# Performance work log

Measured on AMD Instinct MI355X. Metric: run time of the kernel, lower is better.

Reference implementation:

```python
import jax, jax.numpy as jnp
import numpy as np

VOCAB = 50257
D = 256
N_BUBBLES = 64
N_EQ_STEPS = 5
SEQ_LEN = 1024
ETA = 0.1          # relaxation rate of the equilibrium solve
EPS = 1e-10        # eigenvalue clamp for the output distribution


def setup_inputs() -> dict:
    key = jax.random.key(0)
    k1, k2, k3 = jax.random.split(key, 3)
    tokens = jax.random.randint(k1, (SEQ_LEN,), 0, VOCAB)
    embed = jax.random.normal(k2, (VOCAB, D), dtype=jnp.float32) * 0.02
    bubbles = jax.random.normal(k3, (N_BUBBLES, D), dtype=jnp.float32)
    memory_decay = jnp.asarray(0.8, dtype=jnp.float32)
    return {"tokens": tokens, "embed": embed, "bubbles": bubbles,
            "memory_decay": memory_decay}


def _foam_step(memory, x, bubbles, decay):
    # memory: [N_BUBBLES, D], x: [D]
    x_with_memory = x + decay * memory.mean(axis=0)            # [D]
    # equilibrium solve: fixed small number of relaxation iterations
    s = bubbles                                                # [N_BUBBLES, D]
    for _ in range(N_EQ_STEPS):
        mean_field = s.mean(axis=0, keepdims=True)             # [1, D]
        s = s + ETA * (x_with_memory[None, :] - s) + ETA * (mean_field - s)
    # density matrix from equilibrium bubble states
    rho = (s.T @ s) / N_BUBBLES                                # [D, D]
    rho = rho / jnp.trace(rho)
    evals = jnp.linalg.eigvalsh(rho)                           # [D]
    dist = jnp.clip(evals, EPS)
    dist = dist / dist.sum()
    surface_tension = ((s - s.mean(axis=0, keepdims=True)) ** 2).mean()
    memory_new = decay * memory + (1.0 - decay) * s
    return memory_new, dist, surface_tension


def reference(tokens, embed, bubbles, memory_decay):
    decay = jax.nn.sigmoid(memory_decay)
    xs = embed[tokens]                                         # [SEQ_LEN, D]

    def scan_fn(mem, x):
        mem, dist, st = _foam_step(mem, x, bubbles, decay)
        return mem, (dist, st)

    mem0 = jnp.zeros((N_BUBBLES, D), dtype=jnp.float32)
    _, (dists, sts) = jax.lax.scan(scan_fn, mem0, xs)
    # per-step eigenvalue distributions of rho: [SEQ_LEN, D]
    return dists
```

## Files before the change

kernel.cpp:

```cpp
#include <hip/hip_runtime.h>
#include <hip/hip_bf16.h>
#include <math.h>

#define N_B   64
#define DIM   256
#define SEQ   1024
#define CF    0.32768f
#define CF2   0.1073741824f
#define BETA  0.59049f
#define EPSC  1e-10f
#define NSWEEP 3
#define ROUNDS (NSWEEP*63)

#define OFF_BMEAN 16
#define OFF_DT    (OFF_BMEAN + DIM)
#define OFF_DDT   (OFF_DT + DIM*N_B)
#define OFF_M     (OFF_DDT + N_B*N_B)

__global__ __launch_bounds__(256) void prep_kernel(const float* __restrict__ bubbles,
                                                   const float* __restrict__ mdecay,
                                                   float* __restrict__ ws) {
    int d = threadIdx.x;
    float s = 0.f;
    for (int b = 0; b < N_B; ++b) s += bubbles[b*DIM + d];
    float bm = s * (1.f/64.f);
    ws[OFF_BMEAN + d] = bm;
    float sq = 0.f;
    for (int b = 0; b < N_B; ++b) {
        float v = bubbles[b*DIM + d] - bm;
        ws[OFF_DT + d*N_B + b] = v;
        sq += v*v;
    }
    __shared__ float red[256];
    red[d] = sq;
    __syncthreads();
    for (int o = 128; o > 0; o >>= 1) {
        if (d < o) red[d] += red[d+o];
        __syncthreads();
    }
    if (d == 0) {
        ws[1] = red[0];
        ws[0] = 1.f/(1.f + expf(-mdecay[0]));
    }
}

__global__ __launch_bounds__(64) void ddt_kernel(float* __restrict__ ws) {
    const float* Dt = ws + OFF_DT;
    int i = blockIdx.x, j = threadIdx.x;
    __shared__ float coli[DIM];
    #pragma unroll
    for (int kk = 0; kk < 4; ++kk) coli[j + 64*kk] = Dt[(j + 64*kk)*N_B + i];
    __syncthreads();
    float acc = 0.f;
    #pragma unroll 8
    for (int k = 0; k < DIM; ++k) acc += coli[k] * Dt[k*N_B + j];
    ws[OFF_DDT + i*64 + j] = acc;
}

__global__ __launch_bounds__(256) void scan_kernel(const int* __restrict__ tokens,
                                                   const float* __restrict__ embed,
                                                   float* __restrict__ ws) {
    int d = threadIdx.x;
    float decay = ws[0];
    float bm = ws[OFF_BMEAN + d];
    const float omd = 1.f - decay;
    const float omb = 1.f - BETA;
    float mu = 0.f;
    for (int t0 = 0; t0 < SEQ; t0 += 16) {
        float x[16];
        #pragma unroll
        for (int u = 0; u < 16; ++u)
            x[u] = embed[tokens[t0+u]*DIM + d];
        #pragma unroll
        for (int u = 0; u < 16; ++u) {
            float xwm = x[u] + decay*mu;
            float m = BETA*bm + omb*xwm;
            ws[OFF_M + (t0+u)*DIM + d] = m;
            mu = decay*mu + omd*m;
        }
    }
}

__device__ __forceinline__ int triaddr(int i, int j) {
    int mn = min(i, j), mx = max(i, j);
    return mn*65 + mx;
}

__device__ __forceinline__ void tri_decomp(int L, int& a, int& b) {
    int a_ = 0, S = 0;
    while (S + (31 - a_) <= L) { S += 31 - a_; ++a_; }
    a = a_; b = a_ + 1 + (L - S);
}

#define SLOT_INIT(k, p, q, f) { f = ((k) == 0); p = f ? 63 : (k); q = f ? 0 : (63 - (k)); }
#define SLOT_ADV(p, q, f)     { if (!(f)) p = (p == 62) ? 0 : p + 1; q = (q == 62) ? 0 : q + 1; }

__global__ __launch_bounds__(256) void step_kernel(const float* __restrict__ ws,
                                                   float* __restrict__ out) {
    const int t    = blockIdx.x;
    const int tid  = threadIdx.x;
    const int lane = tid & 63;
    const int w    = tid >> 6;

    __shared__ float A[64][65];
    __shared__ float yv[64];
    __shared__ float ml[DIM];
    __shared__ float2 cs[32];
    __shared__ float ypart[4][64];
    __shared__ float wpart[4];
    __shared__ float sorted[64];

    float* Ad = &A[0][0];
    const float* Dt  = ws + OFF_DT;
    const float* DDT = ws + OFF_DDT;
    const float* m   = ws + OFF_M + (size_t)t*DIM;

    float mv = m[tid];
    ml[tid] = mv;
    float pp = mv*mv;
    #pragma unroll
    for (int o = 1; o < 64; o <<= 1) pp += __shfl_xor(pp, o);
    if (lane == 0) wpart[w] = pp;
    __syncthreads();
    const float mm2 = wpart[0]+wpart[1]+wpart[2]+wpart[3];

    {
        float acc = 0.f;
        const float* DtB = Dt + (w*64)*N_B + lane;
        #pragma unroll 8
        for (int kk = 0; kk < 64; ++kk) acc += DtB[kk*N_B] * ml[w*64 + kk];
        ypart[w][lane] = acc;
    }
    __syncthreads();
    if (tid < 64) yv[tid] = ypart[0][tid]+ypart[1][tid]+ypart[2][tid]+ypart[3][tid];
    __syncthreads();

    const float trDD = ws[1];
    const float tr   = mm2 + (CF2/64.f)*trDD;
    const float inv  = 1.f/(64.f*tr);

    {
        int i  = tid >> 2;
        int jb = (tid & 3) * 16;
        const float4* dd = (const float4*)(DDT + i*64 + jb);
        float yi = yv[i];
        #pragma unroll
        for (int u = 0; u < 4; ++u) {
            float4 d4 = dd[u];
            int j = jb + u*4;
            A[i][j+0] = (mm2 + CF*(yi + yv[j+0]) + CF2*d4.x) * inv;
            A[i][j+1] = (mm2 + CF*(yi + yv[j+1]) + CF2*d4.y) * inv;
            A[i][j+2] = (mm2 + CF*(yi + yv[j+2]) + CF2*d4.z) * inv;
            A[i][j+3] = (mm2 + CF*(yi + yv[j+3]) + CF2*d4.w) * inv;
        }
    }
    __syncthreads();

    const bool active = (tid < 248);

    int kr0 = 0, kc0 = 1, kr1 = 0, kc1 = 1;
    if (active) { tri_decomp(2*tid, kr0, kc0); tri_decomp(2*tid+1, kr1, kc1); }

    int pr0, qr0, pc0, qc0, pr1, qr1, pc1, qc1;
    bool fr0, fc0, fr1, fc1;
    SLOT_INIT(kr0, pr0, qr0, fr0);
    SLOT_INIT(kc0, pc0, qc0, fc0);
    SLOT_INIT(kr1, pr1, qr1, fr1);
    SLOT_INIT(kc1, pc1, qc1, fc1);

    int pA = 63, qA = 0; bool fA;
    if (tid < 32) SLOT_INIT(tid, pA, qA, fA);

    for (int rr = 0; rr < ROUNDS; ++rr) {
        if (tid < 32) {
            int aqp = triaddr(pA, qA);
            float app = Ad[pA*65 + pA];
            float aqq = Ad[qA*65 + qA];
            float apq = Ad[aqp];
            float ccf = 1.f, ssf = 0.f, ttf = 0.f;
            if (fabsf(apq) > 1e-36f) {
                float tau = (aqq - app)/(2.f*apq);
                ttf = 1.f/(fabsf(tau) + sqrtf(1.f + tau*tau));
                if (tau < 0.f) ttf = -ttf;
                ccf = rsqrtf(1.f + ttf*ttf);
                ssf = ttf*ccf;
            }
            cs[tid] = make_float2(ccf, ssf);
            Ad[pA*65 + pA] = app - ttf*apq;
            Ad[qA*65 + qA] = aqq + ttf*apq;
            Ad[aqp] = 0.f;
        }
        __syncthreads();

        if (active) {
            {
                float2 cr = cs[kr0], cc2 = cs[kc0];
                int a00 = triaddr(pr0, pc0), a01 = triaddr(pr0, qc0);
                int a10 = triaddr(qr0, pc0), a11 = triaddr(qr0, qc0);
                float x00 = Ad[a00], x01 = Ad[a01], x10 = Ad[a10], x11 = Ad[a11];
                float t0x = cc2.x*x00 - cc2.y*x01, t0y = cc2.y*x00 + cc2.x*x01;
                float t1x = cc2.x*x10 - cc2.y*x11, t1y = cc2.y*x10 + cc2.x*x11;
                Ad[a00] = cr.x*t0x - cr.y*t1x;
                Ad[a01] = cr.x*t0y - cr.y*t1y;
                Ad[a10] = cr.y*t0x + cr.x*t1x;
                Ad[a11] = cr.y*t0y + cr.x*t1y;
            }
            {
                float2 cr = cs[kr1], cc2 = cs[kc1];
                int a00 = triaddr(pr1, pc1), a01 = triaddr(pr1, qc1);
                int a10 = triaddr(qr1, pc1), a11 = triaddr(qr1, qc1);
                float x00 = Ad[a00], x01 = Ad[a01], x10 = Ad[a10], x11 = Ad[a11];
                float t0x = cc2.x*x00 - cc2.y*x01, t0y = cc2.y*x00 + cc2.x*x01;
                float t1x = cc2.x*x10 - cc2.y*x11, t1y = cc2.y*x10 + cc2.x*x11;
                Ad[a00] = cr.x*t0x - cr.y*t1x;
                Ad[a01] = cr.x*t0y - cr.y*t1y;
                Ad[a10] = cr.y*t0x + cr.x*t1x;
                Ad[a11] = cr.y*t0y + cr.x*t1y;
            }
        }

        SLOT_ADV(pr0, qr0, fr0);
        SLOT_ADV(pc0, qc0, fc0);
        SLOT_ADV(pr1, qr1, fr1);
        SLOT_ADV(pc1, qc1, fc1);
        if (tid < 32) SLOT_ADV(pA, qA, fA);
        __syncthreads();
    }

    if (tid < 64) {
        float v = A[tid][tid];
        #pragma unroll
        for (int k = 2; k <= 64; k <<= 1) {
            #pragma unroll
            for (int j = k >> 1; j > 0; j >>= 1) {
                float other = __shfl_xor(v, j);
                bool up    = ((tid & k) == 0);
                bool lower = ((tid & j) == 0);
                v = (lower == up) ? fminf(v, other) : fmaxf(v, other);
            }
        }
        sorted[tid] = v;
    }
    __syncthreads();

    const float invS = 1.f/(1.f + 192.f*EPSC);
    out[(size_t)t*DIM + tid] = (tid < 192) ? EPSC*invS
                                           : fmaxf(sorted[tid-192], EPSC)*invS;
}

extern "C" void kernel_launch(void* const* d_in, const int* in_sizes, int n_in,
                              void* d_out, int out_size, void* d_ws, size_t ws_size,
                              hipStream_t stream) {
    const int*   tokens  = (const int*)d_in[0];
    const float* embed   = (const float*)d_in[1];
    const float* bubbles = (const float*)d_in[2];
    const float* mdecay  = (const float*)d_in[3];
    float* out = (float*)d_out;
    float* ws  = (float*)d_ws;

    hipLaunchKernelGGL(prep_kernel, dim3(1),    dim3(256), 0, stream, bubbles, mdecay, ws);
    hipLaunchKernelGGL(ddt_kernel,  dim3(64),   dim3(64),  0, stream, ws);
    hipLaunchKernelGGL(scan_kernel, dim3(1),    dim3(256), 0, stream, tokens, embed, ws);
    hipLaunchKernelGGL(step_kernel, dim3(1024), dim3(256), 0, stream, ws, out);
}
```

Measured before the change: 363.0 us.

## Prediagonalize shared DDT once and run a single Jacobi sweep per step

Adds a one-time Jacobi eigendecomposition of the token-independent DDT matrix in a new mid_kernel, storing Q, the diagonalized R0 and column sums of Q. The scan runs concurrently in a second block of the same kernel. Each step then builds A in the eigenbasis of DDT, where it is near-diagonal apart from rank-two terms, and cuts the per-step Jacobi work from three sweeps to one. This removes most of the 1024 per-step eigen solves' cost, but a single sweep may not fully converge, which risks eigenvalue accuracy.

```diff
diff --git a/kernel.cpp b/kernel.cpp
--- a/kernel.cpp
+++ b/kernel.cpp
@@ -9,13 +9,17 @@
 #define CF2   0.1073741824f
 #define BETA  0.59049f
 #define EPSC  1e-10f
-#define NSWEEP 3
-#define ROUNDS (NSWEEP*63)
+#define NSWEEP_Q 3
+#define ROUNDS_Q (NSWEEP_Q*63)
+#define ROUNDS_STEP 63
 
 #define OFF_BMEAN 16
 #define OFF_DT    (OFF_BMEAN + DIM)
 #define OFF_DDT   (OFF_DT + DIM*N_B)
-#define OFF_M     (OFF_DDT + N_B*N_B)
+#define OFF_Q     (OFF_DDT + N_B*N_B)
+#define OFF_R0    (OFF_Q + N_B*N_B)
+#define OFF_U     (OFF_R0 + N_B*N_B)
+#define OFF_M     (OFF_U + 64)
 
 __global__ __launch_bounds__(256) void prep_kernel(const float* __restrict__ bubbles,
                                                    const float* __restrict__ mdecay,
@@ -57,30 +61,6 @@
     ws[OFF_DDT + i*64 + j] = acc;
 }
 
-__global__ __launch_bounds__(256) void scan_kernel(const int* __restrict__ tokens,
-                                                   const float* __restrict__ embed,
-                                                   float* __restrict__ ws) {
-    int d = threadIdx.x;
-    float decay = ws[0];
-    float bm = ws[OFF_BMEAN + d];
-    const float omd = 1.f - decay;
-    const float omb = 1.f - BETA;
-    float mu = 0.f;
-    for (int t0 = 0; t0 < SEQ; t0 += 16) {
-        float x[16];
-        #pragma unroll
-        for (int u = 0; u < 16; ++u)
-            x[u] = embed[tokens[t0+u]*DIM + d];
-        #pragma unroll
-        for (int u = 0; u < 16; ++u) {
-            float xwm = x[u] + decay*mu;
-            float m = BETA*bm + omb*xwm;
-            ws[OFF_M + (t0+u)*DIM + d] = m;
-            mu = decay*mu + omd*m;
-        }
-    }
-}
-
 __device__ __forceinline__ int triaddr(int i, int j) {
     int mn = min(i, j), mx = max(i, j);
     return mn*65 + mx;
@@ -95,83 +75,68 @@
 #define SLOT_INIT(k, p, q, f) { f = ((k) == 0); p = f ? 63 : (k); q = f ? 0 : (63 - (k)); }
 #define SLOT_ADV(p, q, f)     { if (!(f)) p = (p == 62) ? 0 : p + 1; q = (q == 62) ? 0 : q + 1; }
 
-__global__ __launch_bounds__(256) void step_kernel(const float* __restrict__ ws,
-                                                   float* __restrict__ out) {
-    const int t    = blockIdx.x;
-    const int tid  = threadIdx.x;
-    const int lane = tid & 63;
-    const int w    = tid >> 6;
+__global__ __launch_bounds__(256) void mid_kernel(const int* __restrict__ tokens,
+                                                  const float* __restrict__ embed,
+                                                  float* __restrict__ ws) {
+    const int tid = threadIdx.x;
+    if (blockIdx.x == 1) {
+        int d = tid;
+        float decay = ws[0];
+        float bm = ws[OFF_BMEAN + d];
+        const float omd = 1.f - decay;
+        const float omb = 1.f - BETA;
+        float mu = 0.f;
+        for (int t0 = 0; t0 < SEQ; t0 += 16) {
+            float x[16];
+            #pragma unroll
+            for (int u = 0; u < 16; ++u)
+                x[u] = embed[tokens[t0+u]*DIM + d];
+            #pragma unroll
+            for (int u = 0; u < 16; ++u) {
+                float xwm = x[u] + decay*mu;
+                float m = BETA*bm + omb*xwm;
+                ws[OFF_M + (t0+u)*DIM + d] = m;
+                mu = decay*mu + omd*m;
+            }
+        }
+        return;
+    }
 
     __shared__ float A[64][65];
-    __shared__ float yv[64];
-    __shared__ float ml[DIM];
+    __shared__ float Qm[64][65];
     __shared__ float2 cs[32];
-    __shared__ float ypart[4][64];
-    __shared__ float wpart[4];
-    __shared__ float sorted[64];
-
     float* Ad = &A[0][0];
-    const float* Dt  = ws + OFF_DT;
-    const float* DDT = ws + OFF_DDT;
-    const float* m   = ws + OFF_M + (size_t)t*DIM;
-
-    float mv = m[tid];
-    ml[tid] = mv;
-    float pp = mv*mv;
-    #pragma unroll
-    for (int o = 1; o < 64; o <<= 1) pp += __shfl_xor(pp, o);
-    if (lane == 0) wpart[w] = pp;
-    __syncthreads();
-    const float mm2 = wpart[0]+wpart[1]+wpart[2]+wpart[3];
 
     {
-        float acc = 0.f;
-        const float* DtB = Dt + (w*64)*N_B + lane;
-        #pragma unroll 8
-        for (int kk = 0; kk < 64; ++kk) acc += DtB[kk*N_B] * ml[w*64 + kk];
-        ypart[w][lane] = acc;
-    }
-    __syncthreads();
-    if (tid < 64) yv[tid] = ypart[0][tid]+ypart[1][tid]+ypart[2][tid]+ypart[3][tid];
-    __syncthreads();
-
-    const float trDD = ws[1];
-    const float tr   = mm2 + (CF2/64.f)*trDD;
-    const float inv  = 1.f/(64.f*tr);
-
-    {
+        const float* DDT = ws + OFF_DDT;
         int i  = tid >> 2;
         int jb = (tid & 3) * 16;
-        const float4* dd = (const float4*)(DDT + i*64 + jb);
-        float yi = yv[i];
         #pragma unroll
-        for (int u = 0; u < 4; ++u) {
-            float4 d4 = dd[u];
-            int j = jb + u*4;
-            A[i][j+0] = (mm2 + CF*(yi + yv[j+0]) + CF2*d4.x) * inv;
-            A[i][j+1] = (mm2 + CF*(yi + yv[j+1]) + CF2*d4.y) * inv;
-            A[i][j+2] = (mm2 + CF*(yi + yv[j+2]) + CF2*d4.z) * inv;
-            A[i][j+3] = (mm2 + CF*(yi + yv[j+3]) + CF2*d4.w) * inv;
+        for (int jj = 0; jj < 16; ++jj) {
+            int j = jb + jj;
+            A[i][j]  = DDT[i*64 + j];
+            Qm[i][j] = (i == j) ? 1.f : 0.f;
         }
     }
     __syncthreads();
 
     const bool active = (tid < 248);
-
     int kr0 = 0, kc0 = 1, kr1 = 0, kc1 = 1;
     if (active) { tri_decomp(2*tid, kr0, kc0); tri_decomp(2*tid+1, kr1, kc1); }
-
     int pr0, qr0, pc0, qc0, pr1, qr1, pc1, qc1;
     bool fr0, fc0, fr1, fc1;
     SLOT_INIT(kr0, pr0, qr0, fr0);
     SLOT_INIT(kc0, pc0, qc0, fc0);
     SLOT_INIT(kr1, pr1, qr1, fr1);
     SLOT_INIT(kc1, pc1, qc1, fc1);
-
     int pA = 63, qA = 0; bool fA;
     if (tid < 32) SLOT_INIT(tid, pA, qA, fA);
-
-    for (int rr = 0; rr < ROUNDS; ++rr) {
+    const int kq = tid & 31;
+    const int qg = (tid >> 5) * 8;
+    int pQ, qQ; bool fQ;
+    SLOT_INIT(kq, pQ, qQ, fQ);
+
+    for (int rr = 0; rr < ROUNDS_Q; ++rr) {
         if (tid < 32) {
             int aqp = triaddr(pA, qA);
             float app = Ad[pA*65 + pA];
@@ -218,6 +183,177 @@
                 Ad[a11] = cr.y*t0y + cr.x*t1y;
             }
         }
+        {
+            float2 cq = cs[kq];
+            #pragma unroll
+            for (int j = 0; j < 8; ++j) {
+                int r = qg + j;
+                float x = Qm[r][pQ], z = Qm[r][qQ];
+                Qm[r][pQ] = cq.x*x - cq.y*z;
+                Qm[r][qQ] = cq.y*x + cq.x*z;
+            }
+        }
+
+        SLOT_ADV(pr0, qr0, fr0);
+        SLOT_ADV(pc0, qc0, fc0);
+        SLOT_ADV(pr1, qr1, fr1);
+        SLOT_ADV(pc1, qc1, fc1);
+        if (tid < 32) SLOT_ADV(pA, qA, fA);
+        SLOT_ADV(pQ, qQ, fQ);
+        __syncthreads();
+    }
+
+    {
+        int i  = tid >> 2;
+        int jb = (tid & 3) * 16;
+        #pragma unroll
+        for (int jj = 0; jj < 16; ++jj) {
+            int j = jb + jj;
+            ws[OFF_R0 + i*64 + j] = CF2 * Ad[triaddr(i, j)];
+            ws[OFF_Q  + i*64 + j] = Qm[i][j];
+        }
+    }
+    if (tid < 64) {
+        float acc = 0.f;
+        #pragma unroll 8
+        for (int r = 0; r < 64; ++r) acc += Qm[r][tid];
+        ws[OFF_U + tid] = acc;
+    }
+}
+
+__global__ __launch_bounds__(256) void step_kernel(const float* __restrict__ ws,
+                                                   float* __restrict__ out) {
+    const int t    = blockIdx.x;
+    const int tid  = threadIdx.x;
+    const int lane = tid & 63;
+    const int w    = tid >> 6;
+
+    __shared__ float A[64][65];
+    __shared__ float yv[64];
+    __shared__ float wv[64];
+    __shared__ float uL[64];
+    __shared__ float ml[DIM];
+    __shared__ float2 cs[32];
+    __shared__ float ypart[4][64];
+    __shared__ float wpart[4];
+    __shared__ float sorted[64];
+
+    float* Ad = &A[0][0];
+    const float* Dt = ws + OFF_DT;
+    const float* m  = ws + OFF_M + (size_t)t*DIM;
+
+    float mv = m[tid];
+    ml[tid] = mv;
+    float pp = mv*mv;
+    #pragma unroll
+    for (int o = 1; o < 64; o <<= 1) pp += __shfl_xor(pp, o);
+    if (lane == 0) wpart[w] = pp;
+    __syncthreads();
+    const float mm2 = wpart[0]+wpart[1]+wpart[2]+wpart[3];
+
+    {
+        float acc = 0.f;
+        const float* DtB = Dt + (w*64)*N_B + lane;
+        #pragma unroll 8
+        for (int kk = 0; kk < 64; ++kk) acc += DtB[kk*N_B] * ml[w*64 + kk];
+        ypart[w][lane] = acc;
+    }
+    __syncthreads();
+    if (tid < 64) yv[tid] = ypart[0][tid]+ypart[1][tid]+ypart[2][tid]+ypart[3][tid];
+    __syncthreads();
+
+    {
+        float acc = 0.f;
+        const float* Qg = ws + OFF_Q + (w*16)*64 + lane;
+        #pragma unroll
+        for (int jj = 0; jj < 16; ++jj) acc += Qg[jj*64] * yv[w*16 + jj];
+        ypart[w][lane] = acc;
+    }
+    if (tid >= 64 && tid < 128) uL[tid-64] = ws[OFF_U + tid-64];
+    __syncthreads();
+    if (tid < 64) wv[tid] = ypart[0][tid]+ypart[1][tid]+ypart[2][tid]+ypart[3][tid];
+    __syncthreads();
+
+    const float trDD = ws[1];
+    const float tr   = mm2 + (CF2/64.f)*trDD;
+    const float inv  = 1.f/(64.f*tr);
+
+    {
+        int i  = tid >> 2;
+        int jb = (tid & 3) * 16;
+        const float4* r4p = (const float4*)(ws + OFF_R0 + i*64 + jb);
+        float ui = uL[i], wi = wv[i];
+        #pragma unroll
+        for (int u4 = 0; u4 < 4; ++u4) {
+            float4 r4 = r4p[u4];
+            int j = jb + u4*4;
+            A[i][j+0] = (r4.x + mm2*ui*uL[j+0] + CF*(ui*wv[j+0] + wi*uL[j+0])) * inv;
+            A[i][j+1] = (r4.y + mm2*ui*uL[j+1] + CF*(ui*wv[j+1] + wi*uL[j+1])) * inv;
+            A[i][j+2] = (r4.z + mm2*ui*uL[j+2] + CF*(ui*wv[j+2] + wi*uL[j+2])) * inv;
+            A[i][j+3] = (r4.w + mm2*ui*uL[j+3] + CF*(ui*wv[j+3] + wi*uL[j+3])) * inv;
+        }
+    }
+    __syncthreads();
+
+    const bool active = (tid < 248);
+    int kr0 = 0, kc0 = 1, kr1 = 0, kc1 = 1;
+    if (active) { tri_decomp(2*tid, kr0, kc0); tri_decomp(2*tid+1, kr1, kc1); }
+    int pr0, qr0, pc0, qc0, pr1, qr1, pc1, qc1;
+    bool fr0, fc0, fr1, fc1;
+    SLOT_INIT(kr0, pr0, qr0, fr0);
+    SLOT_INIT(kc0, pc0, qc0, fc0);
+    SLOT_INIT(kr1, pr1, qr1, fr1);
+    SLOT_INIT(kc1, pc1, qc1, fc1);
+    int pA = 63, qA = 0; bool fA;
+    if (tid < 32) SLOT_INIT(tid, pA, qA, fA);
+
+    for (int rr = 0; rr < ROUNDS_STEP; ++rr) {
+        if (tid < 32) {
+            int aqp = triaddr(pA, qA);
+            float app = Ad[pA*65 + pA];
+            float aqq = Ad[qA*65 + qA];
+            float apq = Ad[aqp];
+            float ccf = 1.f, ssf = 0.f, ttf = 0.f;
+            if (fabsf(apq) > 1e-36f) {
+                float tau = (aqq - app)/(2.f*apq);
+                ttf = 1.f/(fabsf(tau) + sqrtf(1.f + tau*tau));
+                if (tau < 0.f) ttf = -ttf;
+                ccf = rsqrtf(1.f + ttf*ttf);
+                ssf = ttf*ccf;
+            }
+            cs[tid] = make_float2(ccf, ssf);
+            Ad[pA*65 + pA] = app - ttf*apq;
+            Ad[qA*65 + qA] = aqq + ttf*apq;
+            Ad[aqp] = 0.f;
+        }
+        __syncthreads();
+
+        if (active) {
+            {
+                float2 cr = cs[kr0], cc2 = cs[kc0];
+                int a00 = triaddr(pr0, pc0), a01 = triaddr(pr0, qc0);
+                int a10 = triaddr(qr0, pc0), a11 = triaddr(qr0, qc0);
+                float x00 = Ad[a00], x01 = Ad[a01], x10 = Ad[a10], x11 = Ad[a11];
+                float t0x = cc2.x*x00 - cc2.y*x01, t0y = cc2.y*x00 + cc2.x*x01;
+                float t1x = cc2.x*x10 - cc2.y*x11, t1y = cc2.y*x10 + cc2.x*x11;
+                Ad[a00] = cr.x*t0x - cr.y*t1x;
+                Ad[a01] = cr.x*t0y - cr.y*t1y;
+                Ad[a10] = cr.y*t0x + cr.x*t1x;
+                Ad[a11] = cr.y*t0y + cr.x*t1y;
+            }
+            {
+                float2 cr = cs[kr1], cc2 = cs[kc1];
+                int a00 = triaddr(pr1, pc1), a01 = triaddr(pr1, qc1);
+                int a10 = triaddr(qr1, pc1), a11 = triaddr(qr1, qc1);
+                float x00 = Ad[a00], x01 = Ad[a01], x10 = Ad[a10], x11 = Ad[a11];
+                float t0x = cc2.x*x00 - cc2.y*x01, t0y = cc2.y*x00 + cc2.x*x01;
+                float t1x = cc2.x*x10 - cc2.y*x11, t1y = cc2.y*x10 + cc2.x*x11;
+                Ad[a00] = cr.x*t0x - cr.y*t1x;
+                Ad[a01] = cr.x*t0y - cr.y*t1y;
+                Ad[a10] = cr.y*t0x + cr.x*t1x;
+                Ad[a11] = cr.y*t0y + cr.x*t1y;
+            }
+        }
 
         SLOT_ADV(pr0, qr0, fr0);
         SLOT_ADV(pc0, qc0, fc0);
@@ -260,6 +396,6 @@
 
     hipLaunchKernelGGL(prep_kernel, dim3(1),    dim3(256), 0, stream, bubbles, mdecay, ws);
     hipLaunchKernelGGL(ddt_kernel,  dim3(64),   dim3(64),  0, stream, ws);
-    hipLaunchKernelGGL(scan_kernel, dim3(1),    dim3(256), 0, stream, tokens, embed, ws);
+    hipLaunchKernelGGL(mid_kernel,  dim3(2),    dim3(256), 0, stream, tokens, embed, ws);
     hipLaunchKernelGGL(step_kernel, dim3(1024), dim3(256), 0, stream, ws, out);
 }
```

New measurement: 393.6 us. 8.5% more time.
